# Kernel optimization log

Hardware: AMD Instinct MI355X
Metric: run time of the kernel (lower is better)

The kernel has to match this reference:

```python
import jax, jax.numpy as jnp
import numpy as np

B, S, EMBED = 8, 2048, 512
FFN = 2048
N_QUBITS = 10
DEPTH = 2


def _apply_1q(state, mats, wire):
    # state: (N,) + (2,)*n complex; mats: (N,2,2) per-token or (2,2) shared
    s = jnp.moveaxis(state, 1 + wire, 1)
    shp = s.shape
    s = s.reshape(shp[0], 2, -1)
    if mats.ndim == 3:
        s = jnp.einsum('nab,nbr->nar', mats, s)
    else:
        s = jnp.einsum('ab,nbr->nar', mats, s)
    return jnp.moveaxis(s.reshape(shp), 1, 1 + wire)


def _cnot(state, ctrl, tgt):
    # CNOT: flip target axis on the control=1 slice
    ca, ta = 1 + ctrl, 1 + tgt
    s0 = jax.lax.index_in_dim(state, 0, axis=ca, keepdims=True)
    s1 = jax.lax.index_in_dim(state, 1, axis=ca, keepdims=True)
    s1 = jnp.flip(s1, axis=ta)
    return jnp.concatenate([s0, s1], axis=ca)


def _qlayer(x_flat, theta, n_qubits=N_QUBITS, depth=DEPTH):
    # x_flat: (N, n_qubits) RX encoding angles; theta: (n_qubits,) RY params
    N = x_flat.shape[0]
    state = jnp.zeros((N,) + (2,) * n_qubits, jnp.complex64)
    state = state.at[(slice(None),) + (0,) * n_qubits].set(1.0)
    # encoder: RX(x_i) on wire i, per-token angles
    for w in range(n_qubits):
        a = x_flat[:, w] * 0.5
        c = jnp.cos(a).astype(jnp.complex64)
        s = (-1j * jnp.sin(a)).astype(jnp.complex64)
        mats = jnp.stack([jnp.stack([c, s], -1), jnp.stack([s, c], -1)], -2)  # (N,2,2)
        state = _apply_1q(state, mats, w)
    # trainable RY(theta_w) on each wire (shared across tokens)
    for w in range(n_qubits):
        a = theta[w] * 0.5
        c, s = jnp.cos(a), jnp.sin(a)
        mat = jnp.stack([jnp.stack([c, -s]), jnp.stack([s, c])]).astype(jnp.complex64)
        state = _apply_1q(state, mat, w)
    # depth rounds of ring CNOT chain
    for _ in range(depth):
        for w in range(n_qubits - 1):
            state = _cnot(state, w, w + 1)
        state = _cnot(state, n_qubits - 1, 0)
    # MeasureAll PauliZ: <Z_w> per wire
    probs = jnp.abs(state.reshape(N, -1)) ** 2  # (N, 2^n)
    bits = (jnp.arange(2 ** n_qubits)[None, :] >> (n_qubits - 1 - jnp.arange(n_qubits))[:, None]) & 1
    z = (1 - 2 * bits).astype(probs.dtype)  # (n, 2^n)
    return probs @ z.T  # (N, n)


def setup_inputs() -> dict:
    key = jax.random.key(0)
    k = jax.random.split(key, 6)
    x = jax.random.normal(k[0], (B, S, EMBED), jnp.float32)
    ry_theta = jax.random.uniform(k[1], (N_QUBITS,), jnp.float32, 0.0, 2.0 * np.pi)
    W1 = jax.random.normal(k[2], (FFN, N_QUBITS), jnp.float32) / np.sqrt(N_QUBITS)
    b1 = jax.random.normal(k[3], (FFN,), jnp.float32) * 0.01
    W2 = jax.random.normal(k[4], (EMBED, FFN), jnp.float32) / np.sqrt(FFN)
    b2 = jax.random.normal(k[5], (EMBED,), jnp.float32) * 0.01
    return {"x": x, "ry_theta": ry_theta, "W1": W1, "b1": b1, "W2": W2, "b2": b2}


def reference(x, ry_theta, W1, b1, W2, b2):
    b, s, _ = x.shape
    xf = x.reshape(b * s, -1)[:, :N_QUBITS]  # encoder only uses first n_qubits feats
    q = _qlayer(xf, ry_theta).reshape(b, s, N_QUBITS)
    # dropout is identity at eval; linear1 -> relu -> linear2
    h = jax.nn.relu(q @ W1.T + b1)
    return h @ W2.T + b2
```

## Files before the change

### kernel.cpp

```cpp
#include <hip/hip_runtime.h>
#include <hip/hip_bf16.h>


typedef __attribute__((ext_vector_type(8))) short bf16x8;
typedef __attribute__((ext_vector_type(16))) float f32x16;
typedef __attribute__((ext_vector_type(8))) unsigned short us8;
typedef unsigned int u32;

#define NTOK  16384
#define EMBED 512
#define FFN   2048
#define NQ    10
#define BM    128
#define BN    128

__device__ __forceinline__ unsigned short f2bf(float f) {
  union { float f; unsigned int u; } a; a.f = f;
  unsigned int r = a.u + 0x7FFFu + ((a.u >> 16) & 1u);
  return (unsigned short)(r >> 16);
}

__global__ __launch_bounds__(256) void k_cvt_w2f(const float* __restrict__ W2,
                                                 unsigned short* __restrict__ W2f) {
  int gid = blockIdx.x * 256 + threadIdx.x;
  int l = gid & 63, kb = (gid >> 6) & 127, tile = gid >> 13;
  int col = tile * 32 + (l & 31);
  int k0 = kb * 16 + (l >> 5) * 8;
  const float* src = W2 + (size_t)col * FFN + k0;
  float4 v0 = *(const float4*)src;
  float4 v1 = *(const float4*)(src + 4);
  us8 o;
  o[0] = f2bf(v0.x); o[1] = f2bf(v0.y); o[2] = f2bf(v0.z); o[3] = f2bf(v0.w);
  o[4] = f2bf(v1.x); o[5] = f2bf(v1.y); o[6] = f2bf(v1.z); o[7] = f2bf(v1.w);
  *(us8*)(W2f + (size_t)gid * 8) = o;
}

__global__ __launch_bounds__(256) void k_cvt_w1f(const float* __restrict__ W1,
                                                 const float* __restrict__ b1,
                                                 unsigned short* __restrict__ W1f) {
  int gid = blockIdx.x * 256 + threadIdx.x;
  int l = gid & 63, blk = gid >> 6;
  int k = blk * 32 + (l & 31);
  int wg = (l >> 5) * 8;
  us8 o;
#pragma unroll
  for (int e = 0; e < 8; ++e) {
    int wire = wg + e;
    float v = (wire < NQ) ? W1[k * NQ + wire] : (wire == NQ ? b1[k] : 0.f);
    o[e] = f2bf(v);
  }
  *(us8*)(W1f + (size_t)gid * 8) = o;
}

__global__ __launch_bounds__(256) void k_q(const float* __restrict__ x,
                                           const float* __restrict__ theta,
                                           unsigned short* __restrict__ Qf) {
  int gid = blockIdx.x * 256 + threadIdx.x;
  int l = gid & 63, tile = gid >> 6;
  int tok = tile * 32 + (l & 31), g = l >> 5;
  const int masks[NQ] = {0x2AB,0x3FD,0x3FA,0x3F5,0x3EA,0x3D5,0x3AA,0x355,0x2AA,0x155};
  float z[NQ], qv[NQ];
#pragma unroll
  for (int w = 0; w < NQ; ++w)
    z[w] = __builtin_cosf(x[(size_t)tok * EMBED + w]) * __builtin_cosf(theta[w]);
#pragma unroll
  for (int w = 0; w < NQ; ++w) {
    float p = 1.f;
#pragma unroll
    for (int v = 0; v < NQ; ++v)
      if ((masks[w] >> v) & 1) p *= z[v];
    qv[w] = p;
  }
  us8 o = (us8)0;
  if (g == 0) {
#pragma unroll
    for (int e = 0; e < 8; ++e) o[e] = f2bf(qv[e]);
  } else {
    o[0] = f2bf(qv[8]); o[1] = f2bf(qv[9]); o[2] = f2bf(1.f);
  }
  *(us8*)(Qf + (size_t)gid * 8) = o;
}

__global__ __launch_bounds__(256, 2) void k_fused(const unsigned short* __restrict__ Qf,
                                                  const unsigned short* __restrict__ W1f,
                                                  const unsigned short* __restrict__ W2f,
                                                  const float* __restrict__ b2,
                                                  float* __restrict__ out) {
  int bid = blockIdx.x;
  int swz = (bid & 7) * 64 + (bid >> 3);
  const int m0 = (swz >> 2) * BM;
  const int n0 = (swz & 3) * BN;
  const int tid  = threadIdx.x;
  const int lane = tid & 63;
  const int wave = tid >> 6;
  const int wm = wave >> 1, wn = wave & 1;
  const int h = lane >> 5, t31 = lane & 31;

  bf16x8 qf[2];
#pragma unroll
  for (int i = 0; i < 2; ++i)
    qf[i] = *(const bf16x8*)&Qf[(((size_t)(m0 >> 5) + wm * 2 + i) * 64 + lane) * 8];

  f32x16 acc[2][2] = {};
  bf16x8 wfE[2], wfO[2];
  bf16x8 aqA[2][2][2], aqB[2][2][2];
  bf16x8 bgA[8], bgB[8];

#define WLOAD(KT, WF)                                                           \
  { _Pragma("unroll")                                                           \
    for (int b = 0; b < 2; ++b)                                                 \
      WF[b] = *(const bf16x8*)&W1f[(((size_t)(KT) * 2 + b) * 64 + lane) * 8]; }

#define BGLOAD(P, HF, BG)                                                       \
  { _Pragma("unroll")                                                           \
    for (int r = 0; r < 8; ++r) {                                               \
      int j = r >> 2, s = r & 3;                                                \
      int tile = (n0 >> 5) + wn * 2 + j;                                        \
      int kb = (P) * 8 + (HF) * 4 + s;                                          \
      BG[r] = *(const bf16x8*)&W2f[(((size_t)tile * 128 + kb) * 64 + lane) * 8]; \
    } }

#define HGEN(AQ, WF)                                                            \
  { _Pragma("unroll")                                                           \
    for (int i = 0; i < 2; ++i) {                                               \
      _Pragma("unroll")                                                         \
      for (int b = 0; b < 2; ++b) {                                             \
        f32x16 zz = {};                                                         \
        f32x16 d = __builtin_amdgcn_mfma_f32_32x32x16_bf16(WF[b], qf[i], zz, 0, 0, 0); \
        u32 dw0, dw1, dw2, dw3, dw4, dw5, dw6, dw7;                             \
        { float a0=fmaxf(d[0],0.f),a1=fmaxf(d[1],0.f);                          \
          asm("v_cvt_pk_bf16_f32 %0, %1, %2":"=v"(dw0):"v"(a0),"v"(a1)); }      \
        { float a0=fmaxf(d[2],0.f),a1=fmaxf(d[3],0.f);                          \
          asm("v_cvt_pk_bf16_f32 %0, %1, %2":"=v"(dw1):"v"(a0),"v"(a1)); }      \
        { float a0=fmaxf(d[4],0.f),a1=fmaxf(d[5],0.f);                          \
          asm("v_cvt_pk_bf16_f32 %0, %1, %2":"=v"(dw2):"v"(a0),"v"(a1)); }      \
        { float a0=fmaxf(d[6],0.f),a1=fmaxf(d[7],0.f);                          \
          asm("v_cvt_pk_bf16_f32 %0, %1, %2":"=v"(dw3):"v"(a0),"v"(a1)); }      \
        { float a0=fmaxf(d[8],0.f),a1=fmaxf(d[9],0.f);                          \
          asm("v_cvt_pk_bf16_f32 %0, %1, %2":"=v"(dw4):"v"(a0),"v"(a1)); }      \
        { float a0=fmaxf(d[10],0.f),a1=fmaxf(d[11],0.f);                        \
          asm("v_cvt_pk_bf16_f32 %0, %1, %2":"=v"(dw5):"v"(a0),"v"(a1)); }      \
        { float a0=fmaxf(d[12],0.f),a1=fmaxf(d[13],0.f);                        \
          asm("v_cvt_pk_bf16_f32 %0, %1, %2":"=v"(dw6):"v"(a0),"v"(a1)); }      \
        { float a0=fmaxf(d[14],0.f),a1=fmaxf(d[15],0.f);                        \
          asm("v_cvt_pk_bf16_f32 %0, %1, %2":"=v"(dw7):"v"(a0),"v"(a1)); }      \
        asm("v_permlane32_swap_b32 %0, %1" : "+v"(dw0), "+v"(dw2));             \
        asm("v_permlane32_swap_b32 %0, %1" : "+v"(dw1), "+v"(dw3));             \
        asm("v_permlane32_swap_b32 %0, %1" : "+v"(dw4), "+v"(dw6));             \
        asm("v_permlane32_swap_b32 %0, %1" : "+v"(dw5), "+v"(dw7));             \
        union { u32 u[4]; bf16x8 v; } u0, u1;                                   \
        u0.u[0]=dw0; u0.u[1]=dw1; u0.u[2]=dw2; u0.u[3]=dw3;                     \
        u1.u[0]=dw4; u1.u[1]=dw5; u1.u[2]=dw6; u1.u[3]=dw7;                     \
        AQ[i][b][0] = u0.v; AQ[i][b][1] = u1.v;                                 \
      } } }

#define GEMMKT(AQ, BG)                                                          \
  { __builtin_amdgcn_s_setprio(1);                                              \
    _Pragma("unroll")                                                           \
    for (int s = 0; s < 4; ++s) {                                               \
      acc[0][0] = __builtin_amdgcn_mfma_f32_32x32x16_bf16(AQ[0][s >> 1][s & 1], BG[s],     acc[0][0], 0, 0, 0); \
      acc[0][1] = __builtin_amdgcn_mfma_f32_32x32x16_bf16(AQ[0][s >> 1][s & 1], BG[4 + s], acc[0][1], 0, 0, 0); \
      acc[1][0] = __builtin_amdgcn_mfma_f32_32x32x16_bf16(AQ[1][s >> 1][s & 1], BG[s],     acc[1][0], 0, 0, 0); \
      acc[1][1] = __builtin_amdgcn_mfma_f32_32x32x16_bf16(AQ[1][s >> 1][s & 1], BG[4 + s], acc[1][1], 0, 0, 0); \
    }                                                                           \
    __builtin_amdgcn_s_setprio(0); }

  WLOAD(0, wfE);
  WLOAD(1, wfO);
  BGLOAD(0, 0, bgA);
  HGEN(aqA, wfE);

  for (int p = 0; p < 16; ++p) {
    BGLOAD(p, 1, bgB);
    if (p < 15) WLOAD(2 * p + 2, wfE);
    GEMMKT(aqA, bgA);
    HGEN(aqB, wfO);
    if (p < 15) { BGLOAD(p + 1, 0, bgA); WLOAD(2 * p + 3, wfO); }
    GEMMKT(aqB, bgB);
    if (p < 15) HGEN(aqA, wfE);
  }

#pragma unroll
  for (int j = 0; j < 2; ++j) {
    const int col = n0 + wn * 64 + j * 32 + t31;
    const float bbv = b2[col];
#pragma unroll
    for (int i = 0; i < 2; ++i) {
#pragma unroll
      for (int r = 0; r < 16; ++r) {
        int tok = m0 + wm * 64 + i * 32 + (r & 3) + 8 * (r >> 2) + 4 * h;
        out[(size_t)tok * EMBED + col] = acc[i][j][r] + bbv;
      }
    }
  }
#undef WLOAD
#undef BGLOAD
#undef HGEN
#undef GEMMKT
}

extern "C" void kernel_launch(void* const* d_in, const int* in_sizes, int n_in,
                              void* d_out, int out_size, void* d_ws, size_t ws_size,
                              hipStream_t stream) {
  const float* x     = (const float*)d_in[0];
  const float* theta = (const float*)d_in[1];
  const float* W1    = (const float*)d_in[2];
  const float* b1    = (const float*)d_in[3];
  const float* W2    = (const float*)d_in[4];
  const float* b2    = (const float*)d_in[5];
  float* out = (float*)d_out;

  char* ws = (char*)d_ws;
  unsigned short* W2f = (unsigned short*)ws;
  unsigned short* W1f = (unsigned short*)(ws + (2u << 20));
  unsigned short* Qfg = (unsigned short*)(ws + (2u << 20) + (64u << 10));

  k_cvt_w2f<<<512, 256, 0, stream>>>(W2, W2f);
  k_cvt_w1f<<<16, 256, 0, stream>>>(W1, b1, W1f);
  k_q      <<<128, 256, 0, stream>>>(x, theta, Qfg);
  k_fused  <<<(NTOK / BM) * (EMBED / BN), 256, 0, stream>>>(Qfg, W1f, W2f, b2, out);
}
```

Before: 65.48 us.

## Stage W2/W1 tiles in LDS via async loads, 8-wave blocks, merge prep kernels

The three prep kernels (W2 convert, W1 convert, quantum feature compute) are merged into one launch with block-range dispatch, removing two launch gaps. The fused FFN kernel now uses 512 threads (8 waves, each handling 32 tokens) and stages each k-tile of W2 and W1 into double-buffered shared memory with global_load_lds, so waves share weight loads instead of each fetching them from global memory into registers. This cuts redundant global/L2 traffic and register pressure, allowing higher occupancy. In exchange it adds a block barrier per k-step and drops the register-level software pipelining between GEMM and hidden-generation.

Result: faster. 57.44 us (-12.3%).

```diff
diff --git a/kernel.cpp b/kernel.cpp
--- a/kernel.cpp
+++ b/kernel.cpp
@@ -13,6 +13,7 @@
 #define NQ    10
 #define BM    128
 #define BN    128
+#define NKT   32
 
 __device__ __forceinline__ unsigned short f2bf(float f) {
   union { float f; unsigned int u; } a; a.f = f;
@@ -20,72 +21,82 @@
   return (unsigned short)(r >> 16);
 }
 
-__global__ __launch_bounds__(256) void k_cvt_w2f(const float* __restrict__ W2,
-                                                 unsigned short* __restrict__ W2f) {
-  int gid = blockIdx.x * 256 + threadIdx.x;
-  int l = gid & 63, kb = (gid >> 6) & 127, tile = gid >> 13;
-  int col = tile * 32 + (l & 31);
-  int k0 = kb * 16 + (l >> 5) * 8;
-  const float* src = W2 + (size_t)col * FFN + k0;
-  float4 v0 = *(const float4*)src;
-  float4 v1 = *(const float4*)(src + 4);
-  us8 o;
-  o[0] = f2bf(v0.x); o[1] = f2bf(v0.y); o[2] = f2bf(v0.z); o[3] = f2bf(v0.w);
-  o[4] = f2bf(v1.x); o[5] = f2bf(v1.y); o[6] = f2bf(v1.z); o[7] = f2bf(v1.w);
-  *(us8*)(W2f + (size_t)gid * 8) = o;
-}
-
-__global__ __launch_bounds__(256) void k_cvt_w1f(const float* __restrict__ W1,
-                                                 const float* __restrict__ b1,
-                                                 unsigned short* __restrict__ W1f) {
-  int gid = blockIdx.x * 256 + threadIdx.x;
-  int l = gid & 63, blk = gid >> 6;
-  int k = blk * 32 + (l & 31);
-  int wg = (l >> 5) * 8;
-  us8 o;
-#pragma unroll
-  for (int e = 0; e < 8; ++e) {
-    int wire = wg + e;
-    float v = (wire < NQ) ? W1[k * NQ + wire] : (wire == NQ ? b1[k] : 0.f);
-    o[e] = f2bf(v);
+__device__ __forceinline__ void gload_lds16(const void* g, void* l) {
+  __builtin_amdgcn_global_load_lds(
+      (const __attribute__((address_space(1))) unsigned int*)g,
+      (__attribute__((address_space(3))) unsigned int*)l, 16, 0, 0);
+}
+
+__global__ __launch_bounds__(256) void k_prep(const float* __restrict__ x,
+                                              const float* __restrict__ theta,
+                                              const float* __restrict__ W1,
+                                              const float* __restrict__ b1,
+                                              const float* __restrict__ W2,
+                                              unsigned short* __restrict__ W2f,
+                                              unsigned short* __restrict__ W1f,
+                                              unsigned short* __restrict__ Qf) {
+  int bb = blockIdx.x;
+  if (bb < 512) {
+    int gid = bb * 256 + threadIdx.x;
+    int l = gid & 63, kb = (gid >> 6) & 127, tile = gid >> 13;
+    int col = tile * 32 + (l & 31);
+    int k0 = kb * 16 + (l >> 5) * 8;
+    const float* src = W2 + (size_t)col * FFN + k0;
+    float4 v0 = *(const float4*)src;
+    float4 v1 = *(const float4*)(src + 4);
+    us8 o;
+    o[0] = f2bf(v0.x); o[1] = f2bf(v0.y); o[2] = f2bf(v0.z); o[3] = f2bf(v0.w);
+    o[4] = f2bf(v1.x); o[5] = f2bf(v1.y); o[6] = f2bf(v1.z); o[7] = f2bf(v1.w);
+    *(us8*)(W2f + (size_t)gid * 8) = o;
+  } else if (bb < 640) {
+    int gid = (bb - 512) * 256 + threadIdx.x;
+    int l = gid & 63, tile = gid >> 6;
+    int tok = tile * 32 + (l & 31), g = l >> 5;
+    const int masks[NQ] = {0x2AB,0x3FD,0x3FA,0x3F5,0x3EA,0x3D5,0x3AA,0x355,0x2AA,0x155};
+    float z[NQ], qv[NQ];
+#pragma unroll
+    for (int w = 0; w < NQ; ++w)
+      z[w] = __builtin_cosf(x[(size_t)tok * EMBED + w]) * __builtin_cosf(theta[w]);
+#pragma unroll
+    for (int w = 0; w < NQ; ++w) {
+      float p = 1.f;
+#pragma unroll
+      for (int v = 0; v < NQ; ++v)
+        if ((masks[w] >> v) & 1) p *= z[v];
+      qv[w] = p;
+    }
+    us8 o = (us8)0;
+    if (g == 0) {
+#pragma unroll
+      for (int e = 0; e < 8; ++e) o[e] = f2bf(qv[e]);
+    } else {
+      o[0] = f2bf(qv[8]); o[1] = f2bf(qv[9]); o[2] = f2bf(1.f);
+    }
+    *(us8*)(Qf + (size_t)gid * 8) = o;
+  } else {
+    int gid = (bb - 640) * 256 + threadIdx.x;
+    int l = gid & 63, blk = gid >> 6;
+    int k = blk * 32 + (l & 31);
+    int wg = (l >> 5) * 8;
+    us8 o;
+#pragma unroll
+    for (int e = 0; e < 8; ++e) {
+      int wire = wg + e;
+      float v = (wire < NQ) ? W1[k * NQ + wire] : (wire == NQ ? b1[k] : 0.f);
+      o[e] = f2bf(v);
+    }
+    *(us8*)(W1f + (size_t)gid * 8) = o;
   }
-  *(us8*)(W1f + (size_t)gid * 8) = o;
-}
-
-__global__ __launch_bounds__(256) void k_q(const float* __restrict__ x,
-                                           const float* __restrict__ theta,
-                                           unsigned short* __restrict__ Qf) {
-  int gid = blockIdx.x * 256 + threadIdx.x;
-  int l = gid & 63, tile = gid >> 6;
-  int tok = tile * 32 + (l & 31), g = l >> 5;
-  const int masks[NQ] = {0x2AB,0x3FD,0x3FA,0x3F5,0x3EA,0x3D5,0x3AA,0x355,0x2AA,0x155};
-  float z[NQ], qv[NQ];
-#pragma unroll
-  for (int w = 0; w < NQ; ++w)
-    z[w] = __builtin_cosf(x[(size_t)tok * EMBED + w]) * __builtin_cosf(theta[w]);
-#pragma unroll
-  for (int w = 0; w < NQ; ++w) {
-    float p = 1.f;
-#pragma unroll
-    for (int v = 0; v < NQ; ++v)
-      if ((masks[w] >> v) & 1) p *= z[v];
-    qv[w] = p;
-  }
-  us8 o = (us8)0;
-  if (g == 0) {
-#pragma unroll
-    for (int e = 0; e < 8; ++e) o[e] = f2bf(qv[e]);
-  } else {
-    o[0] = f2bf(qv[8]); o[1] = f2bf(qv[9]); o[2] = f2bf(1.f);
-  }
-  *(us8*)(Qf + (size_t)gid * 8) = o;
-}
-
-__global__ __launch_bounds__(256, 2) void k_fused(const unsigned short* __restrict__ Qf,
+}
+
+__global__ __launch_bounds__(512, 4) void k_fused(const unsigned short* __restrict__ Qf,
                                                   const unsigned short* __restrict__ W1f,
                                                   const unsigned short* __restrict__ W2f,
                                                   const float* __restrict__ b2,
                                                   float* __restrict__ out) {
+  __shared__ short Bw[2][16 * 64 * 8];
+  __shared__ short W1s[2][2 * 64 * 8];
+
   int bid = blockIdx.x;
   int swz = (bid & 7) * 64 + (bid >> 3);
   const int m0 = (swz >> 2) * BM;
@@ -95,89 +106,81 @@
   const int wave = tid >> 6;
   const int wm = wave >> 1, wn = wave & 1;
   const int h = lane >> 5, t31 = lane & 31;
-
-  bf16x8 qf[2];
-#pragma unroll
-  for (int i = 0; i < 2; ++i)
-    qf[i] = *(const bf16x8*)&Qf[(((size_t)(m0 >> 5) + wm * 2 + i) * 64 + lane) * 8];
-
-  f32x16 acc[2][2] = {};
-  bf16x8 wfE[2], wfO[2];
-  bf16x8 aqA[2][2][2], aqB[2][2][2];
-  bf16x8 bgA[8], bgB[8];
-
-#define WLOAD(KT, WF)                                                           \
+  const int nt0 = n0 >> 5;
+
+  bf16x8 qf = *(const bf16x8*)&Qf[(((size_t)(m0 >> 5) + wm) * 64 + lane) * 8];
+
+  f32x16 acc[2] = {};
+
+#define STAGE(KT, B)                                                            \
   { _Pragma("unroll")                                                           \
-    for (int b = 0; b < 2; ++b)                                                 \
-      WF[b] = *(const bf16x8*)&W1f[(((size_t)(KT) * 2 + b) * 64 + lane) * 8]; }
-
-#define BGLOAD(P, HF, BG)                                                       \
-  { _Pragma("unroll")                                                           \
-    for (int r = 0; r < 8; ++r) {                                               \
-      int j = r >> 2, s = r & 3;                                                \
-      int tile = (n0 >> 5) + wn * 2 + j;                                        \
-      int kb = (P) * 8 + (HF) * 4 + s;                                          \
-      BG[r] = *(const bf16x8*)&W2f[(((size_t)tile * 128 + kb) * 64 + lane) * 8]; \
-    } }
-
-#define HGEN(AQ, WF)                                                            \
-  { _Pragma("unroll")                                                           \
-    for (int i = 0; i < 2; ++i) {                                               \
-      _Pragma("unroll")                                                         \
-      for (int b = 0; b < 2; ++b) {                                             \
-        f32x16 zz = {};                                                         \
-        f32x16 d = __builtin_amdgcn_mfma_f32_32x32x16_bf16(WF[b], qf[i], zz, 0, 0, 0); \
-        u32 dw0, dw1, dw2, dw3, dw4, dw5, dw6, dw7;                             \
-        { float a0=fmaxf(d[0],0.f),a1=fmaxf(d[1],0.f);                          \
-          asm("v_cvt_pk_bf16_f32 %0, %1, %2":"=v"(dw0):"v"(a0),"v"(a1)); }      \
-        { float a0=fmaxf(d[2],0.f),a1=fmaxf(d[3],0.f);                          \
-          asm("v_cvt_pk_bf16_f32 %0, %1, %2":"=v"(dw1):"v"(a0),"v"(a1)); }      \
-        { float a0=fmaxf(d[4],0.f),a1=fmaxf(d[5],0.f);                          \
-          asm("v_cvt_pk_bf16_f32 %0, %1, %2":"=v"(dw2):"v"(a0),"v"(a1)); }      \
-        { float a0=fmaxf(d[6],0.f),a1=fmaxf(d[7],0.f);                          \
-          asm("v_cvt_pk_bf16_f32 %0, %1, %2":"=v"(dw3):"v"(a0),"v"(a1)); }      \
-        { float a0=fmaxf(d[8],0.f),a1=fmaxf(d[9],0.f);                          \
-          asm("v_cvt_pk_bf16_f32 %0, %1, %2":"=v"(dw4):"v"(a0),"v"(a1)); }      \
-        { float a0=fmaxf(d[10],0.f),a1=fmaxf(d[11],0.f);                        \
-          asm("v_cvt_pk_bf16_f32 %0, %1, %2":"=v"(dw5):"v"(a0),"v"(a1)); }      \
-        { float a0=fmaxf(d[12],0.f),a1=fmaxf(d[13],0.f);                        \
-          asm("v_cvt_pk_bf16_f32 %0, %1, %2":"=v"(dw6):"v"(a0),"v"(a1)); }      \
-        { float a0=fmaxf(d[14],0.f),a1=fmaxf(d[15],0.f);                        \
-          asm("v_cvt_pk_bf16_f32 %0, %1, %2":"=v"(dw7):"v"(a0),"v"(a1)); }      \
-        asm("v_permlane32_swap_b32 %0, %1" : "+v"(dw0), "+v"(dw2));             \
-        asm("v_permlane32_swap_b32 %0, %1" : "+v"(dw1), "+v"(dw3));             \
-        asm("v_permlane32_swap_b32 %0, %1" : "+v"(dw4), "+v"(dw6));             \
-        asm("v_permlane32_swap_b32 %0, %1" : "+v"(dw5), "+v"(dw7));             \
-        union { u32 u[4]; bf16x8 v; } u0, u1;                                   \
-        u0.u[0]=dw0; u0.u[1]=dw1; u0.u[2]=dw2; u0.u[3]=dw3;                     \
-        u1.u[0]=dw4; u1.u[1]=dw5; u1.u[2]=dw6; u1.u[3]=dw7;                     \
-        AQ[i][b][0] = u0.v; AQ[i][b][1] = u1.v;                                 \
-      } } }
-
-#define GEMMKT(AQ, BG)                                                          \
-  { __builtin_amdgcn_s_setprio(1);                                              \
-    _Pragma("unroll")                                                           \
-    for (int s = 0; s < 4; ++s) {                                               \
-      acc[0][0] = __builtin_amdgcn_mfma_f32_32x32x16_bf16(AQ[0][s >> 1][s & 1], BG[s],     acc[0][0], 0, 0, 0); \
-      acc[0][1] = __builtin_amdgcn_mfma_f32_32x32x16_bf16(AQ[0][s >> 1][s & 1], BG[4 + s], acc[0][1], 0, 0, 0); \
-      acc[1][0] = __builtin_amdgcn_mfma_f32_32x32x16_bf16(AQ[1][s >> 1][s & 1], BG[s],     acc[1][0], 0, 0, 0); \
-      acc[1][1] = __builtin_amdgcn_mfma_f32_32x32x16_bf16(AQ[1][s >> 1][s & 1], BG[4 + s], acc[1][1], 0, 0, 0); \
+    for (int hf = 0; hf < 2; ++hf) {                                            \
+      int ch = hf * 512 + tid;                                                  \
+      int tile2 = ch >> 8, kb = (ch >> 6) & 3, ln = ch & 63;                    \
+      gload_lds16(&W2f[(((size_t)(nt0 + tile2) * 128 + (KT) * 4 + kb) * 64 + ln) * 8], \
+                  &Bw[B][ch * 8]);                                              \
     }                                                                           \
-    __builtin_amdgcn_s_setprio(0); }
-
-  WLOAD(0, wfE);
-  WLOAD(1, wfO);
-  BGLOAD(0, 0, bgA);
-  HGEN(aqA, wfE);
-
-  for (int p = 0; p < 16; ++p) {
-    BGLOAD(p, 1, bgB);
-    if (p < 15) WLOAD(2 * p + 2, wfE);
-    GEMMKT(aqA, bgA);
-    HGEN(aqB, wfO);
-    if (p < 15) { BGLOAD(p + 1, 0, bgA); WLOAD(2 * p + 3, wfO); }
-    GEMMKT(aqB, bgB);
-    if (p < 15) HGEN(aqA, wfE);
+    if (tid < 128)                                                              \
+      gload_lds16(&W1f[(((size_t)(KT) * 2 + (tid >> 6)) * 64 + (tid & 63)) * 8],\
+                  &W1s[B][tid * 8]); }
+
+#define HGEN1(WF, AQ0, AQ1)                                                     \
+  { f32x16 zz = {};                                                             \
+    f32x16 d = __builtin_amdgcn_mfma_f32_32x32x16_bf16((WF), qf, zz, 0, 0, 0);  \
+    u32 dw0, dw1, dw2, dw3, dw4, dw5, dw6, dw7;                                 \
+    { float a0=fmaxf(d[0],0.f),a1=fmaxf(d[1],0.f);                              \
+      asm("v_cvt_pk_bf16_f32 %0, %1, %2":"=v"(dw0):"v"(a0),"v"(a1)); }          \
+    { float a0=fmaxf(d[2],0.f),a1=fmaxf(d[3],0.f);                              \
+      asm("v_cvt_pk_bf16_f32 %0, %1, %2":"=v"(dw1):"v"(a0),"v"(a1)); }          \
+    { float a0=fmaxf(d[4],0.f),a1=fmaxf(d[5],0.f);                              \
+      asm("v_cvt_pk_bf16_f32 %0, %1, %2":"=v"(dw2):"v"(a0),"v"(a1)); }          \
+    { float a0=fmaxf(d[6],0.f),a1=fmaxf(d[7],0.f);                              \
+      asm("v_cvt_pk_bf16_f32 %0, %1, %2":"=v"(dw3):"v"(a0),"v"(a1)); }          \
+    { float a0=fmaxf(d[8],0.f),a1=fmaxf(d[9],0.f);                              \
+      asm("v_cvt_pk_bf16_f32 %0, %1, %2":"=v"(dw4):"v"(a0),"v"(a1)); }          \
+    { float a0=fmaxf(d[10],0.f),a1=fmaxf(d[11],0.f);                            \
+      asm("v_cvt_pk_bf16_f32 %0, %1, %2":"=v"(dw5):"v"(a0),"v"(a1)); }          \
+    { float a0=fmaxf(d[12],0.f),a1=fmaxf(d[13],0.f);                            \
+      asm("v_cvt_pk_bf16_f32 %0, %1, %2":"=v"(dw6):"v"(a0),"v"(a1)); }          \
+    { float a0=fmaxf(d[14],0.f),a1=fmaxf(d[15],0.f);                            \
+      asm("v_cvt_pk_bf16_f32 %0, %1, %2":"=v"(dw7):"v"(a0),"v"(a1)); }          \
+    asm("v_permlane32_swap_b32 %0, %1" : "+v"(dw0), "+v"(dw2));                 \
+    asm("v_permlane32_swap_b32 %0, %1" : "+v"(dw1), "+v"(dw3));                 \
+    asm("v_permlane32_swap_b32 %0, %1" : "+v"(dw4), "+v"(dw6));                 \
+    asm("v_permlane32_swap_b32 %0, %1" : "+v"(dw5), "+v"(dw7));                 \
+    union { u32 u[4]; bf16x8 v; } u0, u1;                                       \
+    u0.u[0]=dw0; u0.u[1]=dw1; u0.u[2]=dw2; u0.u[3]=dw3;                         \
+    u1.u[0]=dw4; u1.u[1]=dw5; u1.u[2]=dw6; u1.u[3]=dw7;                         \
+    AQ0 = u0.v; AQ1 = u1.v; }
+
+  STAGE(0, 0);
+
+  for (int kt = 0; kt < NKT; ++kt) {
+    const int cur = kt & 1;
+    asm volatile("s_waitcnt vmcnt(0)" ::: "memory");
+    __builtin_amdgcn_s_barrier();
+    asm volatile("" ::: "memory");
+    if (kt + 1 < NKT) STAGE(kt + 1, cur ^ 1);
+
+    bf16x8 wf0 = *(const bf16x8*)&W1s[cur][(0 * 64 + lane) * 8];
+    bf16x8 wf1 = *(const bf16x8*)&W1s[cur][(1 * 64 + lane) * 8];
+    bf16x8 aq00, aq01, aq10, aq11;
+    HGEN1(wf0, aq00, aq01);
+    HGEN1(wf1, aq10, aq11);
+
+#pragma unroll
+    for (int j = 0; j < 2; ++j) {
+      bf16x8 bg0 = *(const bf16x8*)&Bw[cur][(((wn * 2 + j) * 4 + 0) * 64 + lane) * 8];
+      bf16x8 bg1 = *(const bf16x8*)&Bw[cur][(((wn * 2 + j) * 4 + 1) * 64 + lane) * 8];
+      bf16x8 bg2 = *(const bf16x8*)&Bw[cur][(((wn * 2 + j) * 4 + 2) * 64 + lane) * 8];
+      bf16x8 bg3 = *(const bf16x8*)&Bw[cur][(((wn * 2 + j) * 4 + 3) * 64 + lane) * 8];
+      __builtin_amdgcn_s_setprio(1);
+      acc[j] = __builtin_amdgcn_mfma_f32_32x32x16_bf16(aq00, bg0, acc[j], 0, 0, 0);
+      acc[j] = __builtin_amdgcn_mfma_f32_32x32x16_bf16(aq01, bg1, acc[j], 0, 0, 0);
+      acc[j] = __builtin_amdgcn_mfma_f32_32x32x16_bf16(aq10, bg2, acc[j], 0, 0, 0);
+      acc[j] = __builtin_amdgcn_mfma_f32_32x32x16_bf16(aq11, bg3, acc[j], 0, 0, 0);
+      __builtin_amdgcn_s_setprio(0);
+    }
   }
 
 #pragma unroll
@@ -185,18 +188,13 @@
     const int col = n0 + wn * 64 + j * 32 + t31;
     const float bbv = b2[col];
 #pragma unroll
-    for (int i = 0; i < 2; ++i) {
-#pragma unroll
-      for (int r = 0; r < 16; ++r) {
-        int tok = m0 + wm * 64 + i * 32 + (r & 3) + 8 * (r >> 2) + 4 * h;
-        out[(size_t)tok * EMBED + col] = acc[i][j][r] + bbv;
-      }
+    for (int r = 0; r < 16; ++r) {
+      int tok = m0 + wm * 32 + (r & 3) + 8 * (r >> 2) + 4 * h;
+      out[(size_t)tok * EMBED + col] = acc[j][r] + bbv;
     }
   }
-#undef WLOAD
-#undef BGLOAD
-#undef HGEN
-#undef GEMMKT
+#undef STAGE
+#undef HGEN1
 }
 
 extern "C" void kernel_launch(void* const* d_in, const int* in_sizes, int n_in,
@@ -215,8 +213,6 @@
   unsigned short* W1f = (unsigned short*)(ws + (2u << 20));
   unsigned short* Qfg = (unsigned short*)(ws + (2u << 20) + (64u << 10));
 
-  k_cvt_w2f<<<512, 256, 0, stream>>>(W2, W2f);
-  k_cvt_w1f<<<16, 256, 0, stream>>>(W1, b1, W1f);
-  k_q      <<<128, 256, 0, stream>>>(x, theta, Qfg);
-  k_fused  <<<(NTOK / BM) * (EMBED / BN), 256, 0, stream>>>(Qfg, W1f, W2f, b2, out);
-}
+  k_prep <<<656, 256, 0, stream>>>(x, theta, W1, b1, W2, W2f, W1f, Qfg);
+  k_fused<<<(NTOK / BM) * (EMBED / BN), 512, 0, stream>>>(Qfg, W1f, W2f, b2, out);
+}
```
